# Optimization experiments

Hardware: AMD Instinct MI355X
Metric: run time of the kernel (lower is better)

The kernel has to match this reference:

```python
import jax, jax.numpy as jnp
import numpy as np

EPS = 1e-8  # torch.cosine_similarity eps
TEMPERATURE = 1.0


def setup_inputs() -> dict:
    key = jax.random.key(0)
    ks = jax.random.split(key, 12)
    B = 16384
    inp = {
        "user_ids": jax.random.randint(ks[0], (B, 8), 0, 100000),
        "item_ids": jax.random.randint(ks[1], (B, 4), 0, 50000),
        "sample_weight": jax.random.uniform(ks[2], (B,), jnp.float32, 0.01, 1.0),
        "user_table": jax.random.normal(ks[3], (100000, 64), jnp.float32) * 0.05,
        "item_table": jax.random.normal(ks[4], (50000, 64), jnp.float32) * 0.05,
        "uW1": jax.random.normal(ks[5], (512, 256), jnp.float32) * 0.04,
        "ub1": jnp.zeros((256,), jnp.float32),
        "uW2": jax.random.normal(ks[6], (256, 128), jnp.float32) * 0.06,
        "ub2": jnp.zeros((128,), jnp.float32),
        "iW1": jax.random.normal(ks[7], (256, 256), jnp.float32) * 0.06,
        "ib1": jnp.zeros((256,), jnp.float32),
        "iW2": jax.random.normal(ks[8], (256, 128), jnp.float32) * 0.06,
        "ib2": jnp.zeros((128,), jnp.float32),
        "n_neg": 3,
    }
    return inp


def _tower(ids, table, W1, b1, W2, b2):
    # embedding lookup [B, F, D] -> concat -> [B, F*D], then 2-layer relu MLP
    B = ids.shape[0]
    e = table[ids].reshape(B, -1)
    h = jax.nn.relu(e @ W1 + b1)
    return jax.nn.relu(h @ W2 + b2)


def reference(user_ids, item_ids, sample_weight, user_table, item_table,
              uW1, ub1, uW2, ub2, iW1, ib1, iW2, ib2, n_neg):
    u = _tower(user_ids, user_table, uW1, ub1, uW2, ub2)  # [B, 128]
    v = _tower(item_ids, item_table, iW1, ib1, iW2, ib2)  # [B, 128]
    # cosine similarity per row (torch eps clamp on norms)
    un = jnp.maximum(jnp.linalg.norm(u, axis=1), EPS)
    vn = jnp.maximum(jnp.linalg.norm(v, axis=1), EPS)
    y = jnp.sum(u * v, axis=1) / (un * vn)
    # sampling-bias correction
    y = y - jnp.log(sample_weight)
    # vectorized wrap-around in-batch negative gather:
    # scores[i] = [y[i], y[(i+1)%B], ..., y[(i+n_neg)%B]]
    B = y.shape[0]
    idx = (jnp.arange(B)[:, None] + jnp.arange(n_neg + 1)[None, :]) % B
    scores = y[idx] / TEMPERATURE  # [B, 1+n_neg]
    return scores
```

## Files before the change

### kernel.cpp

```cpp
#include <hip/hip_runtime.h>
#include <math.h>

#define CEPS 1e-8f

typedef __attribute__((ext_vector_type(8))) short bf16x8;
typedef __attribute__((ext_vector_type(4))) float f32x4;
typedef __attribute__((ext_vector_type(4))) unsigned int u32x4;
typedef __attribute__((ext_vector_type(2))) unsigned int u32x2;

__device__ __forceinline__ unsigned short f2bf(float f) {
    unsigned u = __builtin_bit_cast(unsigned, f);
    u += 0x7fffu + ((u >> 16) & 1u);
    return (unsigned short)(u >> 16);
}

__global__ __launch_bounds__(256)
void pack_all(const float* __restrict__ uW1, const float* __restrict__ uW2,
              const float* __restrict__ iW1, const float* __restrict__ iW2,
              unsigned short* __restrict__ o1, unsigned short* __restrict__ o2,
              unsigned short* __restrict__ o3, unsigned short* __restrict__ o4)
{
    int g = blockIdx.x * 256 + threadIdx.x;
    const float* src; unsigned short* dst; int N; int base;
    if (g < 16384)      { src = uW1; dst = o1; N = 256; base = 0;     }
    else if (g < 20480) { src = uW2; dst = o2; N = 128; base = 16384; }
    else if (g < 28672) { src = iW1; dst = o3; N = 256; base = 20480; }
    else                { src = iW2; dst = o4; N = 128; base = 28672; }
    int i = g - base;
    int kg = i / N, n = i - kg * N;
    unsigned short tmp[8];
    #pragma unroll
    for (int j = 0; j < 8; ++j)
        tmp[j] = f2bf(src[(kg * 8 + j) * N + n]);
    *reinterpret_cast<bf16x8*>(dst + ((size_t)i << 3)) =
        *reinterpret_cast<bf16x8*>(tmp);
}


template<int F>
__device__ __forceinline__ void stage_emb(const int* __restrict__ ids,
                                          const float* __restrict__ table,
                                          unsigned short* e_s, int row0, int tid)
{
    constexpr int FC = F * 8;
    constexpr int IT = (64 * FC) / 1024;
    int idv[IT];
    #pragma unroll
    for (int it = 0; it < IT; ++it) {
        int c = tid + it * 1024;
        int r = c / FC, f = (c % FC) >> 3;
        idv[it] = ids[(row0 + r) * F + f];
    }
    #pragma unroll
    for (int it = 0; it < IT; ++it) {
        int c = tid + it * 1024;
        int r = c / FC, rem = c % FC;
        const float* src = table + (size_t)idv[it] * 64 + (rem & 7) * 8;
        float4 aa = *reinterpret_cast<const float4*>(src);
        float4 bb = *reinterpret_cast<const float4*>(src + 4);
        u32x4 pk;
        pk.x = f2bf(aa.x) | ((unsigned)f2bf(aa.y) << 16);
        pk.y = f2bf(aa.z) | ((unsigned)f2bf(aa.w) << 16);
        pk.z = f2bf(bb.x) | ((unsigned)f2bf(bb.y) << 16);
        pk.w = f2bf(bb.z) | ((unsigned)f2bf(bb.w) << 16);
        int byte = r * (F * 128) + rem * 16;
        byte ^= (r & 7) << 4;
        *reinterpret_cast<u32x4*>(reinterpret_cast<char*>(e_s) + byte) = pk;
    }
}

template<int KB>
__device__ __forceinline__ bf16x8 loadA(const unsigned short* s, int ks, int ni,
                                        int l15, int l4)
{
    int row = ni * 16 + l15;
    int byte = row * (KB * 2) + ks * 64 + l4 * 16;
    byte ^= (row & 7) << 4;
    return *reinterpret_cast<const bf16x8*>(
               reinterpret_cast<const char*>(s) + byte);
}

template<int K1>
__device__ __forceinline__ void gemm1(
    const unsigned short* e_s, unsigned short* h_s,
    const unsigned short* __restrict__ W1p, const float* __restrict__ b1,
    int l15, int l4, int wl, const bf16x8* w0)
{
    constexpr int NKS = K1 / 32;
    f32x4 acc[2][4];
    #pragma unroll
    for (int mi = 0; mi < 2; ++mi)
        #pragma unroll
        for (int ni = 0; ni < 4; ++ni) acc[mi][ni] = (f32x4){0.f, 0.f, 0.f, 0.f};

    const unsigned short* Wbase = W1p + ((l4 * 256 + wl * 32 + l15) << 3);
    bf16x8 wf[3][2], ef[2][4];
    wf[0][0] = w0[0];
    wf[0][1] = w0[1];
    #pragma unroll
    for (int mi = 0; mi < 2; ++mi)
        wf[1][mi] = *reinterpret_cast<const bf16x8*>(Wbase + 8192 + (mi << 7));
    #pragma unroll
    for (int ni = 0; ni < 4; ++ni) ef[0][ni] = loadA<K1>(e_s, 0, ni, l15, l4);

    #pragma unroll
    for (int ks = 0; ks < NKS; ++ks) {
        if (ks + 2 < NKS) {
            #pragma unroll
            for (int mi = 0; mi < 2; ++mi)
                wf[(ks + 2) % 3][mi] = *reinterpret_cast<const bf16x8*>(
                    Wbase + (ks + 2) * 8192 + (mi << 7));
        }
        if (ks + 1 < NKS) {
            #pragma unroll
            for (int ni = 0; ni < 4; ++ni)
                ef[(ks + 1) & 1][ni] = loadA<K1>(e_s, ks + 1, ni, l15, l4);
        }
        __builtin_amdgcn_s_setprio(1);
        #pragma unroll
        for (int mi = 0; mi < 2; ++mi)
            #pragma unroll
            for (int ni = 0; ni < 4; ++ni)
                acc[mi][ni] = __builtin_amdgcn_mfma_f32_16x16x32_bf16(
                                  wf[ks % 3][mi], ef[ks & 1][ni], acc[mi][ni], 0, 0, 0);
        __builtin_amdgcn_s_setprio(0);
    }
    float4 bias[2];
    bias[0] = *reinterpret_cast<const float4*>(&b1[wl * 32 + l4 * 4]);
    bias[1] = *reinterpret_cast<const float4*>(&b1[wl * 32 + 16 + l4 * 4]);
    #pragma unroll
    for (int mi = 0; mi < 2; ++mi) {
        const float4 bb = bias[mi];
        #pragma unroll
        for (int ni = 0; ni < 4; ++ni) {
            float v0 = acc[mi][ni][0] + bb.x; v0 = v0 > 0.f ? v0 : 0.f;
            float v1 = acc[mi][ni][1] + bb.y; v1 = v1 > 0.f ? v1 : 0.f;
            float v2 = acc[mi][ni][2] + bb.z; v2 = v2 > 0.f ? v2 : 0.f;
            float v3 = acc[mi][ni][3] + bb.w; v3 = v3 > 0.f ? v3 : 0.f;
            u32x2 d;
            d.x = f2bf(v0) | ((unsigned)f2bf(v1) << 16);
            d.y = f2bf(v2) | ((unsigned)f2bf(v3) << 16);
            int row = ni * 16 + l15;
            int w0c = wl * 32 + mi * 16 + l4 * 4;
            int byte = (row * 256 + w0c) * 2;
            byte ^= (row & 7) << 4;
            *reinterpret_cast<u32x2*>(reinterpret_cast<char*>(h_s) + byte) = d;
        }
    }
}

__device__ __forceinline__ void gemm2(
    const unsigned short* h_s, const unsigned short* __restrict__ W2p,
    f32x4 (&acc)[4], int l15, int l4, int wl, bf16x8 w0)
{
    #pragma unroll
    for (int ni = 0; ni < 4; ++ni) acc[ni] = (f32x4){0.f, 0.f, 0.f, 0.f};

    const unsigned short* Wbase = W2p + ((l4 * 128 + wl * 16 + l15) << 3);
    bf16x8 wf[3], hf[2][4];
    wf[0] = w0;
    wf[1] = *reinterpret_cast<const bf16x8*>(Wbase + 4096);
    #pragma unroll
    for (int ni = 0; ni < 4; ++ni) hf[0][ni] = loadA<256>(h_s, 0, ni, l15, l4);

    #pragma unroll
    for (int ks = 0; ks < 8; ++ks) {
        if (ks + 2 < 8)
            wf[(ks + 2) % 3] = *reinterpret_cast<const bf16x8*>(
                                   Wbase + (ks + 2) * 4096);
        if (ks + 1 < 8) {
            #pragma unroll
            for (int ni = 0; ni < 4; ++ni)
                hf[(ks + 1) & 1][ni] = loadA<256>(h_s, ks + 1, ni, l15, l4);
        }
        __builtin_amdgcn_s_setprio(1);
        #pragma unroll
        for (int ni = 0; ni < 4; ++ni)
            acc[ni] = __builtin_amdgcn_mfma_f32_16x16x32_bf16(
                          wf[ks % 3], hf[ks & 1][ni], acc[ni], 0, 0, 0);
        __builtin_amdgcn_s_setprio(0);
    }
}

__global__ __launch_bounds__(1024, 4)
void fused_sbc(const int* __restrict__ user_ids,  const int* __restrict__ item_ids,
               const float* __restrict__ user_table, const float* __restrict__ item_table,
               const unsigned short* __restrict__ uW1p, const float* __restrict__ ub1,
               const unsigned short* __restrict__ uW2p, const float* __restrict__ ub2,
               const unsigned short* __restrict__ iW1p, const float* __restrict__ ib1,
               const unsigned short* __restrict__ iW2p, const float* __restrict__ ib2,
               const float* __restrict__ sw, float* __restrict__ out,
               int B, int nn1)
{
    __shared__ __align__(16) unsigned short smem[81920];
    unsigned short* e_u = smem;
    unsigned short* e_i = smem + 32768;
    unsigned short* h_u = smem + 49152;
    unsigned short* h_i = smem + 65536;
    float* V_lds = reinterpret_cast<float*>(smem);
    float* red   = reinterpret_cast<float*>(smem + 32768);

    const int tid  = threadIdx.x;
    const int lane = tid & 63;
    const int w    = tid >> 6;
    const int l15  = lane & 15, l4 = lane >> 4;
    const int role = w >> 3;
    const int wl   = w & 7;
    const int row0 = blockIdx.x * 64;

    const unsigned short* W1sel = role ? iW1p : uW1p;
    const unsigned short* W2sel = role ? iW2p : uW2p;

    bf16x8 w0g1[2];
    {
        const unsigned short* base = W1sel + ((l4 * 256 + wl * 32 + l15) << 3);
        w0g1[0] = *reinterpret_cast<const bf16x8*>(base);
        w0g1[1] = *reinterpret_cast<const bf16x8*>(base + 128);
    }
    stage_emb<8>(user_ids, user_table, e_u, row0, tid);
    stage_emb<4>(item_ids, item_table, e_i, row0, tid);
    __syncthreads();

    if (role == 0) gemm1<512>(e_u, h_u, uW1p, ub1, l15, l4, wl, w0g1);
    else           gemm1<256>(e_i, h_i, iW1p, ib1, l15, l4, wl, w0g1);
    bf16x8 w0g2 = *reinterpret_cast<const bf16x8*>(
                      W2sel + ((l4 * 128 + wl * 16 + l15) << 3));
    __syncthreads();

    f32x4 acc2[4];
    if (role == 0) gemm2(h_u, uW2p, acc2, l15, l4, wl, w0g2);
    else           gemm2(h_i, iW2p, acc2, l15, l4, wl, w0g2);

    const int colb = wl * 16 + l4 * 4;

    if (role == 1) {
        const float4 bv = *reinterpret_cast<const float4*>(&ib2[colb]);
        float pv[4];
        #pragma unroll
        for (int ni = 0; ni < 4; ++ni) {
            int row = ni * 16 + l15;
            float v0 = acc2[ni][0] + bv.x; v0 = v0 > 0.f ? v0 : 0.f;
            float v1 = acc2[ni][1] + bv.y; v1 = v1 > 0.f ? v1 : 0.f;
            float v2 = acc2[ni][2] + bv.z; v2 = v2 > 0.f ? v2 : 0.f;
            float v3 = acc2[ni][3] + bv.w; v3 = v3 > 0.f ? v3 : 0.f;
            V_lds[row * 129 + colb + 0] = v0;
            V_lds[row * 129 + colb + 1] = v1;
            V_lds[row * 129 + colb + 2] = v2;
            V_lds[row * 129 + colb + 3] = v3;
            pv[ni] = v0 * v0 + v1 * v1 + v2 * v2 + v3 * v3;
        }
        #pragma unroll
        for (int ni = 0; ni < 4; ++ni) {
            pv[ni] += __shfl_xor(pv[ni], 16);
            pv[ni] += __shfl_xor(pv[ni], 32);
        }
        if (l4 == 0) {
            #pragma unroll
            for (int ni = 0; ni < 4; ++ni)
                red[(wl * 64 + ni * 16 + l15) * 3 + 2] = pv[ni];
        }
    }
    __syncthreads();

    if (role == 0) {
        const float4 bu = *reinterpret_cast<const float4*>(&ub2[colb]);
        float pd[4], pu[4];
        #pragma unroll
        for (int ni = 0; ni < 4; ++ni) {
            int row = ni * 16 + l15;
            float u0 = acc2[ni][0] + bu.x; u0 = u0 > 0.f ? u0 : 0.f;
            float u1 = acc2[ni][1] + bu.y; u1 = u1 > 0.f ? u1 : 0.f;
            float u2 = acc2[ni][2] + bu.z; u2 = u2 > 0.f ? u2 : 0.f;
            float u3 = acc2[ni][3] + bu.w; u3 = u3 > 0.f ? u3 : 0.f;
            float v0 = V_lds[row * 129 + colb + 0];
            float v1 = V_lds[row * 129 + colb + 1];
            float v2 = V_lds[row * 129 + colb + 2];
            float v3 = V_lds[row * 129 + colb + 3];
            pd[ni] = u0 * v0 + u1 * v1 + u2 * v2 + u3 * v3;
            pu[ni] = u0 * u0 + u1 * u1 + u2 * u2 + u3 * u3;
        }
        #pragma unroll
        for (int ni = 0; ni < 4; ++ni) {
            pd[ni] += __shfl_xor(pd[ni], 16);
            pd[ni] += __shfl_xor(pd[ni], 32);
            pu[ni] += __shfl_xor(pu[ni], 16);
            pu[ni] += __shfl_xor(pu[ni], 32);
        }
        if (l4 == 0) {
            #pragma unroll
            for (int ni = 0; ni < 4; ++ni) {
                red[(wl * 64 + ni * 16 + l15) * 3 + 0] = pd[ni];
                red[(wl * 64 + ni * 16 + l15) * 3 + 1] = pu[ni];
            }
        }
    }
    __syncthreads();

    if (tid < 64) {
        int row = tid;
        float d = 0.f, su = 0.f, sv = 0.f;
        #pragma unroll
        for (int cg = 0; cg < 8; ++cg) {
            d  += red[(cg * 64 + row) * 3 + 0];
            su += red[(cg * 64 + row) * 3 + 1];
            sv += red[(cg * 64 + row) * 3 + 2];
        }
        float un = fmaxf(sqrtf(su), CEPS);
        float vn = fmaxf(sqrtf(sv), CEPS);
        int grow = row0 + row;
        float yv = d / (un * vn) - logf(sw[grow]);
        for (int j = 0; j < nn1; ++j) {
            int idx = grow - j;
            if (idx < 0) idx += B;
            out[idx * nn1 + j] = yv;
        }
    }
}

extern "C" void kernel_launch(void* const* d_in, const int* in_sizes, int n_in,
                              void* d_out, int out_size, void* d_ws, size_t ws_size,
                              hipStream_t stream)
{
    const int*   user_ids   = (const int*)  d_in[0];
    const int*   item_ids   = (const int*)  d_in[1];
    const float* sw         = (const float*)d_in[2];
    const float* user_table = (const float*)d_in[3];
    const float* item_table = (const float*)d_in[4];
    const float* uW1        = (const float*)d_in[5];
    const float* ub1        = (const float*)d_in[6];
    const float* uW2        = (const float*)d_in[7];
    const float* ub2        = (const float*)d_in[8];
    const float* iW1        = (const float*)d_in[9];
    const float* ib1        = (const float*)d_in[10];
    const float* iW2        = (const float*)d_in[11];
    const float* ib2        = (const float*)d_in[12];

    const int B   = in_sizes[2];
    const int nn1 = out_size / B;

    unsigned short* wp   = (unsigned short*)d_ws;
    unsigned short* uW1p = wp;
    unsigned short* uW2p = wp + 131072;
    unsigned short* iW1p = wp + 163840;
    unsigned short* iW2p = wp + 229376;
    float* out = (float*)d_out;

    pack_all<<<128, 256, 0, stream>>>(uW1, uW2, iW1, iW2,
                                      uW1p, uW2p, iW1p, iW2p);
    fused_sbc<<<B / 64, 1024, 0, stream>>>(user_ids, item_ids,
                                           user_table, item_table,
                                           uW1p, ub1, uW2p, ub2,
                                           iW1p, ib1, iW2p, ib2,
                                           sw, out, B, nn1);
}
```

Baseline: 28.56 us.

## Halve block row tile to 32 rows with 512 threads and wider per-wave N tiles

Changes the fused kernel from 64 rows per 1024-thread block to 32 rows per 512-thread block, with 4 waves per tower. Each wave now covers 64 output columns in GEMM1 and 32 in GEMM2 across 2 row-subtiles, so weight fragments are reused over fewer rows per wave. LDS use is halved, which allows more resident blocks and doubles the grid. The V exchange also switches to float4 LDS accesses with a 132-float row stride. In exchange, each weight fragment is reused across fewer rows, so total weight traffic from global/L2 doubles.

```diff
diff --git a/kernel.cpp b/kernel.cpp
--- a/kernel.cpp
+++ b/kernel.cpp
@@ -43,17 +43,17 @@
                                           unsigned short* e_s, int row0, int tid)
 {
     constexpr int FC = F * 8;
-    constexpr int IT = (64 * FC) / 1024;
+    constexpr int IT = (32 * FC) / 512;
     int idv[IT];
     #pragma unroll
     for (int it = 0; it < IT; ++it) {
-        int c = tid + it * 1024;
+        int c = tid + it * 512;
         int r = c / FC, f = (c % FC) >> 3;
         idv[it] = ids[(row0 + r) * F + f];
     }
     #pragma unroll
     for (int it = 0; it < IT; ++it) {
-        int c = tid + it * 1024;
+        int c = tid + it * 512;
         int r = c / FC, rem = c % FC;
         const float* src = table + (size_t)idv[it] * 64 + (rem & 7) * 8;
         float4 aa = *reinterpret_cast<const float4*>(src);
@@ -87,52 +87,50 @@
     int l15, int l4, int wl, const bf16x8* w0)
 {
     constexpr int NKS = K1 / 32;
-    f32x4 acc[2][4];
-    #pragma unroll
-    for (int mi = 0; mi < 2; ++mi)
-        #pragma unroll
-        for (int ni = 0; ni < 4; ++ni) acc[mi][ni] = (f32x4){0.f, 0.f, 0.f, 0.f};
-
-    const unsigned short* Wbase = W1p + ((l4 * 256 + wl * 32 + l15) << 3);
-    bf16x8 wf[3][2], ef[2][4];
-    wf[0][0] = w0[0];
-    wf[0][1] = w0[1];
-    #pragma unroll
-    for (int mi = 0; mi < 2; ++mi)
+    f32x4 acc[4][2];
+    #pragma unroll
+    for (int mi = 0; mi < 4; ++mi)
+        #pragma unroll
+        for (int ni = 0; ni < 2; ++ni) acc[mi][ni] = (f32x4){0.f, 0.f, 0.f, 0.f};
+
+    const unsigned short* Wbase = W1p + ((l4 * 256 + wl * 64 + l15) << 3);
+    bf16x8 wf[3][4], ef[2][2];
+    #pragma unroll
+    for (int mi = 0; mi < 4; ++mi) {
+        wf[0][mi] = w0[mi];
         wf[1][mi] = *reinterpret_cast<const bf16x8*>(Wbase + 8192 + (mi << 7));
-    #pragma unroll
-    for (int ni = 0; ni < 4; ++ni) ef[0][ni] = loadA<K1>(e_s, 0, ni, l15, l4);
+    }
+    #pragma unroll
+    for (int ni = 0; ni < 2; ++ni) ef[0][ni] = loadA<K1>(e_s, 0, ni, l15, l4);
 
     #pragma unroll
     for (int ks = 0; ks < NKS; ++ks) {
         if (ks + 2 < NKS) {
             #pragma unroll
-            for (int mi = 0; mi < 2; ++mi)
+            for (int mi = 0; mi < 4; ++mi)
                 wf[(ks + 2) % 3][mi] = *reinterpret_cast<const bf16x8*>(
                     Wbase + (ks + 2) * 8192 + (mi << 7));
         }
         if (ks + 1 < NKS) {
             #pragma unroll
-            for (int ni = 0; ni < 4; ++ni)
+            for (int ni = 0; ni < 2; ++ni)
                 ef[(ks + 1) & 1][ni] = loadA<K1>(e_s, ks + 1, ni, l15, l4);
         }
         __builtin_amdgcn_s_setprio(1);
         #pragma unroll
-        for (int mi = 0; mi < 2; ++mi)
-            #pragma unroll
-            for (int ni = 0; ni < 4; ++ni)
+        for (int mi = 0; mi < 4; ++mi)
+            #pragma unroll
+            for (int ni = 0; ni < 2; ++ni)
                 acc[mi][ni] = __builtin_amdgcn_mfma_f32_16x16x32_bf16(
                                   wf[ks % 3][mi], ef[ks & 1][ni], acc[mi][ni], 0, 0, 0);
         __builtin_amdgcn_s_setprio(0);
     }
-    float4 bias[2];
-    bias[0] = *reinterpret_cast<const float4*>(&b1[wl * 32 + l4 * 4]);
-    bias[1] = *reinterpret_cast<const float4*>(&b1[wl * 32 + 16 + l4 * 4]);
-    #pragma unroll
-    for (int mi = 0; mi < 2; ++mi) {
-        const float4 bb = bias[mi];
-        #pragma unroll
-        for (int ni = 0; ni < 4; ++ni) {
+    #pragma unroll
+    for (int mi = 0; mi < 4; ++mi) {
+        const float4 bb = *reinterpret_cast<const float4*>(
+                              &b1[wl * 64 + mi * 16 + l4 * 4]);
+        #pragma unroll
+        for (int ni = 0; ni < 2; ++ni) {
             float v0 = acc[mi][ni][0] + bb.x; v0 = v0 > 0.f ? v0 : 0.f;
             float v1 = acc[mi][ni][1] + bb.y; v1 = v1 > 0.f ? v1 : 0.f;
             float v2 = acc[mi][ni][2] + bb.z; v2 = v2 > 0.f ? v2 : 0.f;
@@ -141,7 +139,7 @@
             d.x = f2bf(v0) | ((unsigned)f2bf(v1) << 16);
             d.y = f2bf(v2) | ((unsigned)f2bf(v3) << 16);
             int row = ni * 16 + l15;
-            int w0c = wl * 32 + mi * 16 + l4 * 4;
+            int w0c = wl * 64 + mi * 16 + l4 * 4;
             int byte = (row * 256 + w0c) * 2;
             byte ^= (row & 7) << 4;
             *reinterpret_cast<u32x2*>(reinterpret_cast<char*>(h_s) + byte) = d;
@@ -151,38 +149,48 @@
 
 __device__ __forceinline__ void gemm2(
     const unsigned short* h_s, const unsigned short* __restrict__ W2p,
-    f32x4 (&acc)[4], int l15, int l4, int wl, bf16x8 w0)
-{
-    #pragma unroll
-    for (int ni = 0; ni < 4; ++ni) acc[ni] = (f32x4){0.f, 0.f, 0.f, 0.f};
-
-    const unsigned short* Wbase = W2p + ((l4 * 128 + wl * 16 + l15) << 3);
-    bf16x8 wf[3], hf[2][4];
-    wf[0] = w0;
-    wf[1] = *reinterpret_cast<const bf16x8*>(Wbase + 4096);
-    #pragma unroll
-    for (int ni = 0; ni < 4; ++ni) hf[0][ni] = loadA<256>(h_s, 0, ni, l15, l4);
+    f32x4 (&acc)[2][2], int l15, int l4, int wl, const bf16x8* w0)
+{
+    #pragma unroll
+    for (int mi = 0; mi < 2; ++mi)
+        #pragma unroll
+        for (int ni = 0; ni < 2; ++ni) acc[mi][ni] = (f32x4){0.f, 0.f, 0.f, 0.f};
+
+    const unsigned short* Wbase = W2p + ((l4 * 128 + wl * 32 + l15) << 3);
+    bf16x8 wf[3][2], hf[2][2];
+    #pragma unroll
+    for (int mi = 0; mi < 2; ++mi) {
+        wf[0][mi] = w0[mi];
+        wf[1][mi] = *reinterpret_cast<const bf16x8*>(Wbase + 4096 + (mi << 7));
+    }
+    #pragma unroll
+    for (int ni = 0; ni < 2; ++ni) hf[0][ni] = loadA<256>(h_s, 0, ni, l15, l4);
 
     #pragma unroll
     for (int ks = 0; ks < 8; ++ks) {
-        if (ks + 2 < 8)
-            wf[(ks + 2) % 3] = *reinterpret_cast<const bf16x8*>(
-                                   Wbase + (ks + 2) * 4096);
+        if (ks + 2 < 8) {
+            #pragma unroll
+            for (int mi = 0; mi < 2; ++mi)
+                wf[(ks + 2) % 3][mi] = *reinterpret_cast<const bf16x8*>(
+                    Wbase + (ks + 2) * 4096 + (mi << 7));
+        }
         if (ks + 1 < 8) {
             #pragma unroll
-            for (int ni = 0; ni < 4; ++ni)
+            for (int ni = 0; ni < 2; ++ni)
                 hf[(ks + 1) & 1][ni] = loadA<256>(h_s, ks + 1, ni, l15, l4);
         }
         __builtin_amdgcn_s_setprio(1);
         #pragma unroll
-        for (int ni = 0; ni < 4; ++ni)
-            acc[ni] = __builtin_amdgcn_mfma_f32_16x16x32_bf16(
-                          wf[ks % 3], hf[ks & 1][ni], acc[ni], 0, 0, 0);
+        for (int mi = 0; mi < 2; ++mi)
+            #pragma unroll
+            for (int ni = 0; ni < 2; ++ni)
+                acc[mi][ni] = __builtin_amdgcn_mfma_f32_16x16x32_bf16(
+                                  wf[ks % 3][mi], hf[ks & 1][ni], acc[mi][ni], 0, 0, 0);
         __builtin_amdgcn_s_setprio(0);
     }
 }
 
-__global__ __launch_bounds__(1024, 4)
+__global__ __launch_bounds__(512, 4)
 void fused_sbc(const int* __restrict__ user_ids,  const int* __restrict__ item_ids,
                const float* __restrict__ user_table, const float* __restrict__ item_table,
                const unsigned short* __restrict__ uW1p, const float* __restrict__ ub1,
@@ -192,30 +200,31 @@
                const float* __restrict__ sw, float* __restrict__ out,
                int B, int nn1)
 {
-    __shared__ __align__(16) unsigned short smem[81920];
+    __shared__ __align__(16) unsigned short smem[40960];
     unsigned short* e_u = smem;
-    unsigned short* e_i = smem + 32768;
-    unsigned short* h_u = smem + 49152;
-    unsigned short* h_i = smem + 65536;
+    unsigned short* e_i = smem + 16384;
+    unsigned short* h_u = smem + 24576;
+    unsigned short* h_i = smem + 32768;
     float* V_lds = reinterpret_cast<float*>(smem);
-    float* red   = reinterpret_cast<float*>(smem + 32768);
+    float* red   = reinterpret_cast<float*>(smem + 16384);
 
     const int tid  = threadIdx.x;
     const int lane = tid & 63;
     const int w    = tid >> 6;
     const int l15  = lane & 15, l4 = lane >> 4;
-    const int role = w >> 3;
-    const int wl   = w & 7;
-    const int row0 = blockIdx.x * 64;
+    const int role = w >> 2;
+    const int wl   = w & 3;
+    const int row0 = blockIdx.x * 32;
 
     const unsigned short* W1sel = role ? iW1p : uW1p;
     const unsigned short* W2sel = role ? iW2p : uW2p;
 
-    bf16x8 w0g1[2];
+    bf16x8 w0g1[4];
     {
-        const unsigned short* base = W1sel + ((l4 * 256 + wl * 32 + l15) << 3);
-        w0g1[0] = *reinterpret_cast<const bf16x8*>(base);
-        w0g1[1] = *reinterpret_cast<const bf16x8*>(base + 128);
+        const unsigned short* base = W1sel + ((l4 * 256 + wl * 64 + l15) << 3);
+        #pragma unroll
+        for (int mi = 0; mi < 4; ++mi)
+            w0g1[mi] = *reinterpret_cast<const bf16x8*>(base + (mi << 7));
     }
     stage_emb<8>(user_ids, user_table, e_u, row0, tid);
     stage_emb<4>(item_ids, item_table, e_i, row0, tid);
@@ -223,64 +232,70 @@
 
     if (role == 0) gemm1<512>(e_u, h_u, uW1p, ub1, l15, l4, wl, w0g1);
     else           gemm1<256>(e_i, h_i, iW1p, ib1, l15, l4, wl, w0g1);
-    bf16x8 w0g2 = *reinterpret_cast<const bf16x8*>(
-                      W2sel + ((l4 * 128 + wl * 16 + l15) << 3));
+    bf16x8 w0g2[2];
+    {
+        const unsigned short* base = W2sel + ((l4 * 128 + wl * 32 + l15) << 3);
+        w0g2[0] = *reinterpret_cast<const bf16x8*>(base);
+        w0g2[1] = *reinterpret_cast<const bf16x8*>(base + 128);
+    }
     __syncthreads();
 
-    f32x4 acc2[4];
+    f32x4 acc2[2][2];
     if (role == 0) gemm2(h_u, uW2p, acc2, l15, l4, wl, w0g2);
     else           gemm2(h_i, iW2p, acc2, l15, l4, wl, w0g2);
 
-    const int colb = wl * 16 + l4 * 4;
-
     if (role == 1) {
-        const float4 bv = *reinterpret_cast<const float4*>(&ib2[colb]);
-        float pv[4];
-        #pragma unroll
-        for (int ni = 0; ni < 4; ++ni) {
-            int row = ni * 16 + l15;
-            float v0 = acc2[ni][0] + bv.x; v0 = v0 > 0.f ? v0 : 0.f;
-            float v1 = acc2[ni][1] + bv.y; v1 = v1 > 0.f ? v1 : 0.f;
-            float v2 = acc2[ni][2] + bv.z; v2 = v2 > 0.f ? v2 : 0.f;
-            float v3 = acc2[ni][3] + bv.w; v3 = v3 > 0.f ? v3 : 0.f;
-            V_lds[row * 129 + colb + 0] = v0;
-            V_lds[row * 129 + colb + 1] = v1;
-            V_lds[row * 129 + colb + 2] = v2;
-            V_lds[row * 129 + colb + 3] = v3;
-            pv[ni] = v0 * v0 + v1 * v1 + v2 * v2 + v3 * v3;
-        }
-        #pragma unroll
-        for (int ni = 0; ni < 4; ++ni) {
+        float pv[2] = {0.f, 0.f};
+        #pragma unroll
+        for (int mi = 0; mi < 2; ++mi) {
+            const int colb = wl * 32 + mi * 16 + l4 * 4;
+            const float4 bv = *reinterpret_cast<const float4*>(&ib2[colb]);
+            #pragma unroll
+            for (int ni = 0; ni < 2; ++ni) {
+                int row = ni * 16 + l15;
+                float v0 = acc2[mi][ni][0] + bv.x; v0 = v0 > 0.f ? v0 : 0.f;
+                float v1 = acc2[mi][ni][1] + bv.y; v1 = v1 > 0.f ? v1 : 0.f;
+                float v2 = acc2[mi][ni][2] + bv.z; v2 = v2 > 0.f ? v2 : 0.f;
+                float v3 = acc2[mi][ni][3] + bv.w; v3 = v3 > 0.f ? v3 : 0.f;
+                float4 vv = {v0, v1, v2, v3};
+                *reinterpret_cast<float4*>(&V_lds[row * 132 + colb]) = vv;
+                pv[ni] += v0 * v0 + v1 * v1 + v2 * v2 + v3 * v3;
+            }
+        }
+        #pragma unroll
+        for (int ni = 0; ni < 2; ++ni) {
             pv[ni] += __shfl_xor(pv[ni], 16);
             pv[ni] += __shfl_xor(pv[ni], 32);
         }
         if (l4 == 0) {
             #pragma unroll
-            for (int ni = 0; ni < 4; ++ni)
-                red[(wl * 64 + ni * 16 + l15) * 3 + 2] = pv[ni];
+            for (int ni = 0; ni < 2; ++ni)
+                red[(wl * 32 + ni * 16 + l15) * 3 + 2] = pv[ni];
         }
     }
     __syncthreads();
 
     if (role == 0) {
-        const float4 bu = *reinterpret_cast<const float4*>(&ub2[colb]);
-        float pd[4], pu[4];
-        #pragma unroll
-        for (int ni = 0; ni < 4; ++ni) {
-            int row = ni * 16 + l15;
-            float u0 = acc2[ni][0] + bu.x; u0 = u0 > 0.f ? u0 : 0.f;
-            float u1 = acc2[ni][1] + bu.y; u1 = u1 > 0.f ? u1 : 0.f;
-            float u2 = acc2[ni][2] + bu.z; u2 = u2 > 0.f ? u2 : 0.f;
-            float u3 = acc2[ni][3] + bu.w; u3 = u3 > 0.f ? u3 : 0.f;
-            float v0 = V_lds[row * 129 + colb + 0];
-            float v1 = V_lds[row * 129 + colb + 1];
-            float v2 = V_lds[row * 129 + colb + 2];
-            float v3 = V_lds[row * 129 + colb + 3];
-            pd[ni] = u0 * v0 + u1 * v1 + u2 * v2 + u3 * v3;
-            pu[ni] = u0 * u0 + u1 * u1 + u2 * u2 + u3 * u3;
-        }
-        #pragma unroll
-        for (int ni = 0; ni < 4; ++ni) {
+        float pd[2] = {0.f, 0.f}, pu[2] = {0.f, 0.f};
+        #pragma unroll
+        for (int mi = 0; mi < 2; ++mi) {
+            const int colb = wl * 32 + mi * 16 + l4 * 4;
+            const float4 bu = *reinterpret_cast<const float4*>(&ub2[colb]);
+            #pragma unroll
+            for (int ni = 0; ni < 2; ++ni) {
+                int row = ni * 16 + l15;
+                float u0 = acc2[mi][ni][0] + bu.x; u0 = u0 > 0.f ? u0 : 0.f;
+                float u1 = acc2[mi][ni][1] + bu.y; u1 = u1 > 0.f ? u1 : 0.f;
+                float u2 = acc2[mi][ni][2] + bu.z; u2 = u2 > 0.f ? u2 : 0.f;
+                float u3 = acc2[mi][ni][3] + bu.w; u3 = u3 > 0.f ? u3 : 0.f;
+                const float4 vv = *reinterpret_cast<const float4*>(
+                                      &V_lds[row * 132 + colb]);
+                pd[ni] += u0 * vv.x + u1 * vv.y + u2 * vv.z + u3 * vv.w;
+                pu[ni] += u0 * u0 + u1 * u1 + u2 * u2 + u3 * u3;
+            }
+        }
+        #pragma unroll
+        for (int ni = 0; ni < 2; ++ni) {
             pd[ni] += __shfl_xor(pd[ni], 16);
             pd[ni] += __shfl_xor(pd[ni], 32);
             pu[ni] += __shfl_xor(pu[ni], 16);
@@ -288,22 +303,22 @@
         }
         if (l4 == 0) {
             #pragma unroll
-            for (int ni = 0; ni < 4; ++ni) {
-                red[(wl * 64 + ni * 16 + l15) * 3 + 0] = pd[ni];
-                red[(wl * 64 + ni * 16 + l15) * 3 + 1] = pu[ni];
+            for (int ni = 0; ni < 2; ++ni) {
+                red[(wl * 32 + ni * 16 + l15) * 3 + 0] = pd[ni];
+                red[(wl * 32 + ni * 16 + l15) * 3 + 1] = pu[ni];
             }
         }
     }
     __syncthreads();
 
-    if (tid < 64) {
+    if (tid < 32) {
         int row = tid;
         float d = 0.f, su = 0.f, sv = 0.f;
         #pragma unroll
-        for (int cg = 0; cg < 8; ++cg) {
-            d  += red[(cg * 64 + row) * 3 + 0];
-            su += red[(cg * 64 + row) * 3 + 1];
-            sv += red[(cg * 64 + row) * 3 + 2];
+        for (int cg = 0; cg < 4; ++cg) {
+            d  += red[(cg * 32 + row) * 3 + 0];
+            su += red[(cg * 32 + row) * 3 + 1];
+            sv += red[(cg * 32 + row) * 3 + 2];
         }
         float un = fmaxf(sqrtf(su), CEPS);
         float vn = fmaxf(sqrtf(sv), CEPS);
@@ -347,9 +362,9 @@
 
     pack_all<<<128, 256, 0, stream>>>(uW1, uW2, iW1, iW2,
                                       uW1p, uW2p, iW1p, iW2p);
-    fused_sbc<<<B / 64, 1024, 0, stream>>>(user_ids, item_ids,
-                                           user_table, item_table,
-                                           uW1p, ub1, uW2p, ub2,
-                                           iW1p, ib1, iW2p, ib2,
-                                           sw, out, B, nn1);
-}
+    fused_sbc<<<B / 32, 512, 0, stream>>>(user_ids, item_ids,
+                                          user_table, item_table,
+                                          uW1p, ub1, uW2p, ub2,
+                                          iW1p, ib1, iW2p, ib2,
+                                          sw, out, B, nn1);
+}
```

Result: no change. 28.30 us (-0.9%).
